# Kernel tuning notes

Hardware: AMD Instinct MI355X
Metric: run time of the kernel (lower is better)

The kernel has to match this reference:

```python
import jax, jax.numpy as jnp
import numpy as np

B = 4096
HID = 1024
Z1P = 256
Z1R = 256
Z2P = 128
Z2R = 128
N_STEP = 32


def _gru_cell(x, h, Wih, Whh, bih, bhh):
    # torch.nn.GRUCell math. Wih: [3H, in], Whh: [3H, H]
    gi = x @ Wih.T + bih  # [B, 3H]
    gh = h @ Whh.T + bhh  # [B, 3H]
    i_r, i_z, i_n = jnp.split(gi, 3, axis=1)
    h_r, h_z, h_n = jnp.split(gh, 3, axis=1)
    r = jax.nn.sigmoid(i_r + h_r)
    zg = jax.nn.sigmoid(i_z + h_z)
    n = jnp.tanh(i_n + r * h_n)
    return (1.0 - zg) * n + zg * h


def _decode(z, Wi, bi, Wih, Whh, bih, bhh, Wo, bo, out_dim):
    b = z.shape[0]
    h0 = jnp.tanh(z @ Wi.T + bi)  # linear_init + tanh
    out0 = jnp.zeros((b, out_dim), z.dtype).at[:, -1].set(1.0)  # SOS token

    def step(carry, _):
        out, h = carry
        x = jnp.concatenate([out, z], axis=1)  # [B, out_dim + z_dim]
        h = _gru_cell(x, h, Wih, Whh, bih, bhh)
        o = h @ Wo.T + bo  # linear_out
        return (o, h), o

    _, xs = jax.lax.scan(step, (out0, h0), None, length=N_STEP)  # xs: [T, B, out_dim]
    return jnp.transpose(xs, (1, 0, 2))  # [B, T, out_dim]


def setup_inputs() -> dict:
    key = jax.random.key(0)
    ks = jax.random.split(key, 24)
    s = lambda fan_in: 1.0 / np.sqrt(fan_in)
    u = lambda k, shape, fan_in: jax.random.uniform(k, shape, jnp.float32, -s(fan_in), s(fan_in))
    inp = {
        "z_8p": jax.random.normal(ks[0], (B, Z1P), jnp.float32),
        "z_8r": jax.random.normal(ks[1], (B, Z1R), jnp.float32),
        "z_4p": jax.random.normal(ks[2], (B, Z2P), jnp.float32),
        "z_4r": jax.random.normal(ks[3], (B, Z2R), jnp.float32),
        # linear_init_0 / linear_init_1
        "Wi0": u(ks[4], (HID, Z1P), Z1P), "bi0": u(ks[5], (HID,), Z1P),
        "Wi1": u(ks[6], (HID, Z1R), Z1R), "bi1": u(ks[7], (HID,), Z1R),
        # grucell_0 (input = z1p + z2p)
        "Wih0": u(ks[8], (3 * HID, Z1P + Z2P), HID), "Whh0": u(ks[9], (3 * HID, HID), HID),
        "bih0": u(ks[10], (3 * HID,), HID), "bhh0": u(ks[11], (3 * HID,), HID),
        # grucell_1 (input = z1r + z2r)
        "Wih1": u(ks[12], (3 * HID, Z1R + Z2R), HID), "Whh1": u(ks[13], (3 * HID, HID), HID),
        "bih1": u(ks[14], (3 * HID,), HID), "bhh1": u(ks[15], (3 * HID,), HID),
        # linear_out_0 / linear_out_1
        "Wo0": u(ks[16], (Z2P, HID), HID), "bo0": u(ks[17], (Z2P,), HID),
        "Wo1": u(ks[18], (Z2R, HID), HID), "bo1": u(ks[19], (Z2R,), HID),
    }
    return inp


def reference(z_8p, z_8r, z_4p, z_4r,
              Wi0, bi0, Wi1, bi1,
              Wih0, Whh0, bih0, bhh0,
              Wih1, Whh1, bih1, bhh1,
              Wo0, bo0, Wo1, bo1):
    # eval-mode forward; z_4p / z_4r are only cached during training and do not
    # affect the output (teacher-forcing branches in the source are no-ops).
    z4p = _decode(z_8p, Wi0, bi0, Wih0, Whh0, bih0, bhh0, Wo0, bo0, Z2P)
    z4r = _decode(z_8r, Wi1, bi1, Wih1, Whh1, bih1, bhh1, Wo1, bo1, Z2R)
    return (z4p, z4r)
```

## Files before the change

kernel.cpp:

```cpp
#include <hip/hip_runtime.h>
#include <stdint.h>


typedef unsigned short u16;
typedef __attribute__((ext_vector_type(8))) short bf8v;
typedef __attribute__((ext_vector_type(4))) float f4v;

constexpr int DECN = 2;
constexpr int BB = 4096;
constexpr int HH = 1024;
constexpr int ZZ = 256;
constexpr int OO = 128;
constexpr int TT = 32;
constexpr int GG = 3 * HH;
constexpr int WR = 4 * HH + OO;
constexpr int ILD = OO + ZZ;

__device__ __forceinline__ float bf2f(u16 u) {
  uint32_t x = ((uint32_t)u) << 16;
  return __builtin_bit_cast(float, x);
}
__device__ __forceinline__ u16 f2bf(float f) {
  uint32_t x = __builtin_bit_cast(uint32_t, f);
  x += 0x7fffu + ((x >> 16) & 1u);
  return (u16)(x >> 16);
}
__device__ __forceinline__ float sigf(float x) { return 1.f / (1.f + __expf(-x)); }
__device__ __forceinline__ float tanh_fast(float x) { return 2.f / (1.f + __expf(-2.f * x)) - 1.f; }

__device__ __forceinline__ void load16(const u16* g, u16* l) {
  __builtin_amdgcn_global_load_lds(
      (const __attribute__((address_space(1))) unsigned int*)g,
      (__attribute__((address_space(3))) unsigned int*)l, 16, 0, 0);
}

template <int NSEC>
__device__ __forceinline__ void gemm_core(
    const u16* __restrict__ A, int lda,
    const u16* __restrict__ Bm, int ldb,
    const int (&brow)[NSEC], int m0, int K,
    u16* Als, u16* Bls, f4v (&acc)[NSEC][4][2]) {
  const int tid = threadIdx.x;
  const int lane = tid & 63;
  const int wid = tid >> 6;
  const int wm = wid >> 1, wn = wid & 1;
  const int srow = lane >> 2;
  const int scol = (lane & 3) * 8;
  const int l15 = lane & 15;
  const int khalf = (lane >> 4) * 8;

  for (int k0 = 0; k0 < K; k0 += 32) {
    const u16* ga = A + (size_t)(m0 + wid * 16 + srow) * lda + k0 + scol;
    load16(ga, Als + (wid * 16) * 32);
    load16(ga + (size_t)64 * lda, Als + (64 + wid * 16) * 32);
#pragma unroll
    for (int s = 0; s < NSEC; ++s) {
      const u16* gb = Bm + (size_t)(brow[s] + wid * 16 + srow) * ldb + k0 + scol;
      load16(gb, Bls + (s * 64 + wid * 16) * 32);
    }
    __syncthreads();
    bf8v af[4];
#pragma unroll
    for (int mf = 0; mf < 4; ++mf)
      af[mf] = *(const bf8v*)(Als + (wm * 64 + mf * 16 + l15) * 32 + khalf);
#pragma unroll
    for (int s = 0; s < NSEC; ++s) {
#pragma unroll
      for (int nf = 0; nf < 2; ++nf) {
        bf8v bv = *(const bf8v*)(Bls + (s * 64 + wn * 32 + nf * 16 + l15) * 32 + khalf);
#pragma unroll
        for (int mf = 0; mf < 4; ++mf)
          acc[s][mf][nf] = __builtin_amdgcn_mfma_f32_16x16x32_bf16(af[mf], bv, acc[s][mf][nf], 0, 0, 0);
      }
    }
    __syncthreads();
  }
}


__global__ __launch_bounds__(256) void pack_kernel(const float* __restrict__ src, int ld, int col0,
                                                   u16* __restrict__ dst, int rows, int cols) {
  int i = blockIdx.x * 256 + threadIdx.x;
  if (i < rows * cols) {
    int r = i / cols, c = i - r * cols;
    dst[i] = f2bf(src[(size_t)r * ld + col0 + c]);
  }
}

__global__ __launch_bounds__(256) void wot_kernel(const float* __restrict__ wo, u16* __restrict__ dst) {
  int i = blockIdx.x * 256 + threadIdx.x;
  if (i < HH * OO) {
    int k = i / OO, c = i - k * OO;
    dst[i] = f2bf(wo[(size_t)c * HH + k]);
  }
}

__global__ __launch_bounds__(256) void vec_kernel(
    const float* __restrict__ wih0, const float* __restrict__ wih1,
    const float* __restrict__ bih0, const float* __restrict__ bih1,
    const float* __restrict__ bhh0, const float* __restrict__ bhh1,
    const float* __restrict__ bo0, const float* __restrict__ bo1,
    float* __restrict__ d1, float* __restrict__ v2) {
  int i = blockIdx.x * 256 + threadIdx.x;
  if (i >= DECN * GG) return;
  int dec = i / GG, j = i - dec * GG;
  const float* wih = dec ? wih1 : wih0;
  const float* bo = dec ? bo1 : bo0;
  const float* bih = dec ? bih1 : bih0;
  const float* bhh = dec ? bhh1 : bhh0;
  float bc = 0.f;
  for (int c = 0; c < OO; ++c) bc += wih[(size_t)j * ILD + c] * bo[c];
  d1[i] = wih[(size_t)j * ILD + (OO - 1)] - bc;
  v2[i] = bih[j] + (j < 2 * HH ? bhh[j] : 0.f) + bc;
}

__global__ __launch_bounds__(256, 2) void comb_kernel(
    const u16* __restrict__ wio, const u16* __restrict__ wot,
    const float* __restrict__ whh0, const float* __restrict__ whh1,
    u16* __restrict__ wb2) {
  __shared__ u16 Als[128 * 32];
  __shared__ u16 Bls[64 * 32];
  const int dec = blockIdx.z, m0 = blockIdx.x * 128, n0 = blockIdx.y * 64;
  const int lane = threadIdx.x & 63, wid = threadIdx.x >> 6;
  const int wm = wid >> 1, wn = wid & 1;
  const int rbase = m0 + wm * 64 + ((lane >> 4) << 2);
  const int clb = wn * 32 + (lane & 15);
  int brow[1] = {n0};
  f4v acc[1][4][2];
#pragma unroll
  for (int mf = 0; mf < 4; ++mf)
#pragma unroll
    for (int nf = 0; nf < 2; ++nf)
#pragma unroll
      for (int r = 0; r < 4; ++r) acc[0][mf][nf][r] = 0.f;
  gemm_core<1>(wio + (size_t)dec * GG * OO, OO, wot + (size_t)dec * HH * OO, OO, brow, m0, OO, Als, Bls, acc);
  const float* whh = dec ? whh1 : whh0;
  u16* W2 = wb2 + (size_t)dec * WR * HH;
#pragma unroll
  for (int mf = 0; mf < 4; ++mf)
#pragma unroll
    for (int nf = 0; nf < 2; ++nf) {
      const int k = n0 + clb + nf * 16;
#pragma unroll
      for (int r = 0; r < 4; ++r) {
        const int j = rbase + mf * 16 + r;
        float v = acc[0][mf][nf][r] + (j < 2 * HH ? whh[(size_t)j * HH + k] : 0.f);
        W2[(size_t)j * HH + k] = f2bf(v);
      }
    }
}

__global__ __launch_bounds__(256, 2) void gzc_kernel(
    const u16* __restrict__ zbf, const u16* __restrict__ wzb,
    const float* __restrict__ v2, u16* __restrict__ gzc) {
  __shared__ u16 Als[128 * 32];
  __shared__ u16 Bls[64 * 32];
  const int dec = blockIdx.z, m0 = blockIdx.x * 128, n0 = blockIdx.y * 64;
  const int lane = threadIdx.x & 63, wid = threadIdx.x >> 6;
  const int wm = wid >> 1, wn = wid & 1;
  const int rbase = m0 + wm * 64 + ((lane >> 4) << 2);
  const int clb = wn * 32 + (lane & 15);
  int brow[1] = {n0};
  f4v acc[1][4][2];
#pragma unroll
  for (int mf = 0; mf < 4; ++mf)
#pragma unroll
    for (int nf = 0; nf < 2; ++nf)
#pragma unroll
      for (int r = 0; r < 4; ++r) acc[0][mf][nf][r] = 0.f;
  gemm_core<1>(zbf + (size_t)dec * BB * ZZ, ZZ, wzb + (size_t)dec * GG * ZZ, ZZ, brow, m0, ZZ, Als, Bls, acc);
  const float* vv = v2 + dec * GG;
  u16* out = gzc + (size_t)dec * BB * GG;
#pragma unroll
  for (int mf = 0; mf < 4; ++mf)
#pragma unroll
    for (int nf = 0; nf < 2; ++nf) {
      const int col = n0 + clb + nf * 16;
#pragma unroll
      for (int r = 0; r < 4; ++r) {
        const int row = rbase + mf * 16 + r;
        out[(size_t)row * GG + col] = f2bf(acc[0][mf][nf][r] + vv[col]);
      }
    }
}

__global__ __launch_bounds__(256, 2) void h0_kernel(
    const u16* __restrict__ zbf, const u16* __restrict__ wib,
    const float* __restrict__ bi0, const float* __restrict__ bi1,
    float* __restrict__ hf, u16* __restrict__ hbf) {
  __shared__ u16 Als[128 * 32];
  __shared__ u16 Bls[64 * 32];
  const int dec = blockIdx.z, m0 = blockIdx.x * 128, n0 = blockIdx.y * 64;
  const int lane = threadIdx.x & 63, wid = threadIdx.x >> 6;
  const int wm = wid >> 1, wn = wid & 1;
  const int rbase = m0 + wm * 64 + ((lane >> 4) << 2);
  const int clb = wn * 32 + (lane & 15);
  int brow[1] = {n0};
  f4v acc[1][4][2];
#pragma unroll
  for (int mf = 0; mf < 4; ++mf)
#pragma unroll
    for (int nf = 0; nf < 2; ++nf)
#pragma unroll
      for (int r = 0; r < 4; ++r) acc[0][mf][nf][r] = 0.f;
  gemm_core<1>(zbf + (size_t)dec * BB * ZZ, ZZ, wib + (size_t)dec * HH * ZZ, ZZ, brow, m0, ZZ, Als, Bls, acc);
  const float* bi = dec ? bi1 : bi0;
  float* ho = hf + (size_t)dec * 2 * BB * HH;
  u16* hb = hbf + (size_t)dec * 2 * BB * HH;
#pragma unroll
  for (int mf = 0; mf < 4; ++mf)
#pragma unroll
    for (int nf = 0; nf < 2; ++nf) {
      const int col = n0 + clb + nf * 16;
#pragma unroll
      for (int r = 0; r < 4; ++r) {
        const int row = rbase + mf * 16 + r;
        float v = tanh_fast(acc[0][mf][nf][r] + bi[col]);
        ho[(size_t)row * HH + col] = v;
        hb[(size_t)row * HH + col] = f2bf(v);
      }
    }
}

__global__ __launch_bounds__(256, 2) void step_kernel(
    const u16* __restrict__ hbf_in, const float* __restrict__ hf_in,
    float* __restrict__ hf_out, u16* __restrict__ hbf_out,
    const u16* __restrict__ Wb, const u16* __restrict__ gzc,
    const float* __restrict__ d1,
    const float* __restrict__ bhh0v, const float* __restrict__ bhh1v,
    const float* __restrict__ bo0v, const float* __restrict__ bo1v,
    float* __restrict__ dout, int step1, int o_slot, int y_base) {
  __shared__ u16 Als[128 * 32];
  __shared__ u16 Bls[4 * 64 * 32];
  const int dec = blockIdx.z;
  const int ntile = blockIdx.y + y_base;
  const int m0 = blockIdx.x * 128;
  const int lane = threadIdx.x & 63, wid = threadIdx.x >> 6;
  const int wm = wid >> 1, wn = wid & 1;
  const int rbase = m0 + wm * 64 + ((lane >> 4) << 2);
  const int clb = wn * 32 + (lane & 15);
  const u16* A = hbf_in + (size_t)dec * 2 * BB * HH;
  const u16* W = Wb + (size_t)dec * WR * HH;

  if (ntile < 16) {
    const int j0 = ntile * 64;
    int brow[4] = {j0, HH + j0, 2 * HH + j0, 3 * HH + j0};
    const u16* gz = gzc + (size_t)dec * BB * GG;
    const float* dd = d1 + dec * GG;
    const float* bhhn = (dec ? bhh1v : bhh0v) + 2 * HH;
    f4v acc[4][4][2];
#pragma unroll
    for (int mf = 0; mf < 4; ++mf)
#pragma unroll
      for (int nf = 0; nf < 2; ++nf) {
        const int col = j0 + clb + nf * 16;
        const float dr0 = step1 ? dd[col] : 0.f;
        const float dr1 = step1 ? dd[HH + col] : 0.f;
        const float dr2 = step1 ? dd[2 * HH + col] : 0.f;
        const float bn = bhhn[col];
#pragma unroll
        for (int r = 0; r < 4; ++r) {
          const size_t ro = (size_t)(rbase + mf * 16 + r) * GG;
          acc[0][mf][nf][r] = bf2f(gz[ro + col]) + dr0;
          acc[1][mf][nf][r] = bf2f(gz[ro + HH + col]) + dr1;
          acc[2][mf][nf][r] = bf2f(gz[ro + 2 * HH + col]) + dr2;
          acc[3][mf][nf][r] = bn;
        }
      }
    gemm_core<4>(A, HH, W, HH, brow, m0, HH, Als, Bls, acc);
    const float* hold = hf_in + (size_t)dec * 2 * BB * HH;
    float* hnew = hf_out + (size_t)dec * 2 * BB * HH;
    u16* hnb = hbf_out + (size_t)dec * 2 * BB * HH;
#pragma unroll
    for (int mf = 0; mf < 4; ++mf)
#pragma unroll
      for (int nf = 0; nf < 2; ++nf) {
        const int col = j0 + clb + nf * 16;
#pragma unroll
        for (int r = 0; r < 4; ++r) {
          const int row = rbase + mf * 16 + r;
          float rg = sigf(acc[0][mf][nf][r]);
          float zg = sigf(acc[1][mf][nf][r]);
          float nn = tanh_fast(acc[2][mf][nf][r] + rg * acc[3][mf][nf][r]);
          float hv = hold[(size_t)row * HH + col];
          float hn = (1.f - zg) * nn + zg * hv;
          hnew[(size_t)row * HH + col] = hn;
          hnb[(size_t)row * HH + col] = f2bf(hn);
        }
      }
  } else {
    const int c0 = (ntile - 16) * 64;
    int brow[1] = {4 * HH + c0};
    const float* bod = dec ? bo1v : bo0v;
    f4v acc[1][4][2];
#pragma unroll
    for (int mf = 0; mf < 4; ++mf)
#pragma unroll
      for (int nf = 0; nf < 2; ++nf) {
        const float b = bod[c0 + clb + nf * 16];
#pragma unroll
        for (int r = 0; r < 4; ++r) acc[0][mf][nf][r] = b;
      }
    gemm_core<1>(A, HH, W, HH, brow, m0, HH, Als, Bls, acc);
    float* op = dout + (size_t)dec * BB * TT * OO + (size_t)o_slot * OO;
#pragma unroll
    for (int mf = 0; mf < 4; ++mf)
#pragma unroll
      for (int nf = 0; nf < 2; ++nf) {
        const int col = c0 + clb + nf * 16;
#pragma unroll
        for (int r = 0; r < 4; ++r) {
          const int row = rbase + mf * 16 + r;
          op[(size_t)row * TT * OO + col] = acc[0][mf][nf][r];
        }
      }
  }
}


extern "C" void kernel_launch(void* const* d_in, const int* in_sizes, int n_in,
                              void* d_out, int out_size, void* d_ws, size_t ws_size,
                              hipStream_t stream) {
  const float* z8[2] = {(const float*)d_in[0], (const float*)d_in[1]};
  const float* Wi[2] = {(const float*)d_in[4], (const float*)d_in[6]};
  const float* bi[2] = {(const float*)d_in[5], (const float*)d_in[7]};
  const float* Wih[2] = {(const float*)d_in[8], (const float*)d_in[12]};
  const float* Whh[2] = {(const float*)d_in[9], (const float*)d_in[13]};
  const float* bih[2] = {(const float*)d_in[10], (const float*)d_in[14]};
  const float* bhh[2] = {(const float*)d_in[11], (const float*)d_in[15]};
  const float* Wo[2] = {(const float*)d_in[16], (const float*)d_in[18]};
  const float* bo[2] = {(const float*)d_in[17], (const float*)d_in[19]};
  float* dout = (float*)d_out;

  char* p = (char*)d_ws;
  size_t off = 0;
  auto carve = [&](size_t nbytes) {
    char* r = p + off;
    off += (nbytes + 255) & ~(size_t)255;
    return (void*)r;
  };
  float* hf = (float*)carve((size_t)DECN * 2 * BB * HH * 4);
  u16* hbf = (u16*)carve((size_t)DECN * 2 * BB * HH * 2);
  u16* gzc = (u16*)carve((size_t)DECN * BB * GG * 2);
  u16* wb1 = (u16*)carve((size_t)DECN * WR * HH * 2);
  u16* wb2 = (u16*)carve((size_t)DECN * WR * HH * 2);
  u16* zbf = (u16*)carve((size_t)DECN * BB * ZZ * 2);
  u16* wzb = (u16*)carve((size_t)DECN * GG * ZZ * 2);
  u16* wio = (u16*)carve((size_t)DECN * GG * OO * 2);
  u16* wib = (u16*)carve((size_t)DECN * HH * ZZ * 2);
  u16* wot = (u16*)carve((size_t)DECN * HH * OO * 2);
  float* d1v = (float*)carve((size_t)DECN * GG * 4);
  float* v2v = (float*)carve((size_t)DECN * GG * 4);
  (void)ws_size; (void)in_sizes; (void)n_in; (void)out_size;

  auto pack = [&](const float* src, int ld, int c0, u16* dst, int rows, int cols) {
    int n = rows * cols;
    pack_kernel<<<(n + 255) / 256, 256, 0, stream>>>(src, ld, c0, dst, rows, cols);
  };
  for (int d = 0; d < 2; ++d) {
    pack(z8[d], ZZ, 0, zbf + (size_t)d * BB * ZZ, BB, ZZ);
    pack(Wih[d], ILD, OO, wzb + (size_t)d * GG * ZZ, GG, ZZ);
    pack(Wih[d], ILD, 0, wio + (size_t)d * GG * OO, GG, OO);
    pack(Wi[d], ZZ, 0, wib + (size_t)d * HH * ZZ, HH, ZZ);
    pack(Whh[d], HH, 0, wb1 + (size_t)d * WR * HH, 2 * HH, HH);
    pack(Whh[d] + (size_t)2 * HH * HH, HH, 0, wb1 + (size_t)d * WR * HH + (size_t)3 * HH * HH, HH, HH);
    pack(Whh[d] + (size_t)2 * HH * HH, HH, 0, wb2 + (size_t)d * WR * HH + (size_t)3 * HH * HH, HH, HH);
    pack(Wo[d], HH, 0, wb2 + (size_t)d * WR * HH + (size_t)4 * HH * HH, OO, HH);
    wot_kernel<<<(HH * OO + 255) / 256, 256, 0, stream>>>(Wo[d], wot + (size_t)d * HH * OO);
    hipMemsetAsync(wb1 + (size_t)d * WR * HH + (size_t)2 * HH * HH, 0, (size_t)HH * HH * 2, stream);
  }
  vec_kernel<<<(DECN * GG + 255) / 256, 256, 0, stream>>>(
      Wih[0], Wih[1], bih[0], bih[1], bhh[0], bhh[1], bo[0], bo[1], d1v, v2v);
  comb_kernel<<<dim3(24, 16, 2), 256, 0, stream>>>(wio, wot, Whh[0], Whh[1], wb2);
  gzc_kernel<<<dim3(32, 48, 2), 256, 0, stream>>>(zbf, wzb, v2v, gzc);
  h0_kernel<<<dim3(32, 16, 2), 256, 0, stream>>>(zbf, wib, bi[0], bi[1], hf, hbf);

  for (int t = 1; t <= TT; ++t) {
    const int bin = (t - 1) & 1, bout = t & 1;
    dim3 grid(32, t == 1 ? 16 : 18, 2);
    step_kernel<<<grid, 256, 0, stream>>>(
        hbf + (size_t)bin * BB * HH, hf + (size_t)bin * BB * HH,
        hf + (size_t)bout * BB * HH, hbf + (size_t)bout * BB * HH,
        t == 1 ? wb1 : wb2, gzc, d1v, bhh[0], bhh[1], bo[0], bo[1],
        dout, t == 1 ? 1 : 0, t - 2, 0);
  }
  step_kernel<<<dim3(32, 2, 2), 256, 0, stream>>>(
      hbf, hf, hf + (size_t)BB * HH, hbf + (size_t)BB * HH,
      wb2, gzc, d1v, bhh[0], bhh[1], bo[0], bo[1],
      dout, 0, TT - 1, 16);
}
```

Measured before the change: 3.427 ms.

## Replace step GEMM with 256-row, 8-wave, BK=64 double-buffered swizzled MFMA kernel

Replaces the per-step GRU kernel with a new 512-thread kernel that tiles 256 batch rows by four 64-column gate slices, using a 64-wide K tile. The loop double-buffers A and W tiles in LDS through direct global-to-LDS loads with an XOR swizzle. It interleaves prefetch with MFMA work using explicit waitcnt, barriers and setprio. The output projection is merged into one tile covering all 128 columns, and bias and gate-input addition move into the epilogue. This is meant to cut repeated weight and activation loads and raise MFMA utilisation, at the cost of fewer, larger blocks, higher register pressure and hand-tuned synchronisation that could be fragile.

Measured after the change: 3.209 ms. 6.4% less time.

```diff
diff --git a/kernel.cpp b/kernel.cpp
--- a/kernel.cpp
+++ b/kernel.cpp
@@ -15,6 +15,8 @@
 constexpr int GG = 3 * HH;
 constexpr int WR = 4 * HH + OO;
 constexpr int ILD = OO + ZZ;
+constexpr int BK = 64;
+constexpr int NKT = HH / BK;
 
 __device__ __forceinline__ float bf2f(u16 u) {
   uint32_t x = ((uint32_t)u) << 16;
@@ -222,7 +224,84 @@
     }
 }
 
-__global__ __launch_bounds__(256, 2) void step_kernel(
+template <int NS>
+__device__ __forceinline__ void kloop8(
+    const u16* __restrict__ A, const u16* __restrict__ W,
+    const int (&brow)[4], int m0, u16* lds, int lane, int wid,
+    f4v (&acc)[8][4]) {
+  const int wm = wid >> 2, wn = wid & 3;
+  const int l15 = lane & 15, lq = lane >> 4;
+  const int srow = wid * 8 + (lane >> 3);
+  const int sgc = (lane & 7) ^ ((lane >> 3) & 7);
+
+  auto stA = [&](int kt, int r) {
+    const u16* g = A + (size_t)(m0 + r * 64 + srow) * HH + kt * BK + sgc * 8;
+    load16(g, lds + ((kt & 1) * 2) * 16384 + (r * 64 + wid * 8) * 64);
+  };
+  auto stB = [&](int kt, int r) {
+    const u16* g = W + (size_t)(brow[r] + srow) * HH + kt * BK + sgc * 8;
+    load16(g, lds + ((kt & 1) * 2 + 1) * 16384 + (r * 64 + wid * 8) * 64);
+  };
+
+  stB(0, 0); stB(0, 1); stB(0, 2); stB(0, 3);
+  stA(0, 0); stA(0, 1); stA(0, 2); stA(0, 3);
+  asm volatile("s_waitcnt vmcnt(0)" ::: "memory");
+  __builtin_amdgcn_s_barrier();
+
+  auto tile = [&](int kt, bool pf) {
+    const u16* la = lds + (size_t)(kt & 1) * 32768;
+    const u16* lb = la + 16384;
+    bf8v bfr[NS][2];
+#pragma unroll
+    for (int q = 0; q < 4; ++q) {
+      if (q == 0) {
+#pragma unroll
+        for (int s = 0; s < NS; ++s)
+#pragma unroll
+          for (int ks = 0; ks < 2; ++ks)
+            bfr[s][ks] = *(const bf8v*)&lb[(s * 64 + wn * 16 + l15) * 64 +
+                                           (((ks * 4 + lq) ^ (l15 & 7)) * 8)];
+      }
+      bf8v aq[2][2];
+#pragma unroll
+      for (int mi = 0; mi < 2; ++mi)
+#pragma unroll
+        for (int ks = 0; ks < 2; ++ks)
+          aq[mi][ks] = *(const bf8v*)&la[(wm * 128 + (2 * q + mi) * 16 + l15) * 64 +
+                                         (((ks * 4 + lq) ^ (l15 & 7)) * 8)];
+      if (pf) {
+        if (q == 0) { stB(kt + 1, 0); stB(kt + 1, 1); }
+        if (q == 1) { stB(kt + 1, 2); stB(kt + 1, 3); }
+        if (q == 2) { stA(kt + 1, 0); stA(kt + 1, 2); }
+        if (q == 3) { stA(kt + 1, 1); stA(kt + 1, 3); }
+      }
+      __builtin_amdgcn_s_barrier();
+      asm volatile("s_waitcnt lgkmcnt(0)" ::: "memory");
+      __builtin_amdgcn_s_setprio(1);
+#pragma unroll
+      for (int mi = 0; mi < 2; ++mi)
+#pragma unroll
+        for (int s = 0; s < NS; ++s)
+#pragma unroll
+          for (int ks = 0; ks < 2; ++ks)
+            acc[2 * q + mi][s] = __builtin_amdgcn_mfma_f32_16x16x32_bf16(
+                aq[mi][ks], bfr[s][ks], acc[2 * q + mi][s], 0, 0, 0);
+      __builtin_amdgcn_s_setprio(0);
+      if (q == 1) {
+        if (pf) asm volatile("s_waitcnt vmcnt(4)" ::: "memory");
+        else    asm volatile("s_waitcnt vmcnt(0)" ::: "memory");
+      }
+      if (q == 3) {
+        asm volatile("s_waitcnt vmcnt(2)" ::: "memory");
+      }
+      __builtin_amdgcn_s_barrier();
+    }
+  };
+  for (int kt = 0; kt < NKT - 1; ++kt) tile(kt, true);
+  tile(NKT - 1, false);
+}
+
+__global__ __launch_bounds__(512, 2) void step8_kernel(
     const u16* __restrict__ hbf_in, const float* __restrict__ hf_in,
     float* __restrict__ hf_out, u16* __restrict__ hbf_out,
     const u16* __restrict__ Wb, const u16* __restrict__ gzc,
@@ -230,88 +309,73 @@
     const float* __restrict__ bhh0v, const float* __restrict__ bhh1v,
     const float* __restrict__ bo0v, const float* __restrict__ bo1v,
     float* __restrict__ dout, int step1, int o_slot, int y_base) {
-  __shared__ u16 Als[128 * 32];
-  __shared__ u16 Bls[4 * 64 * 32];
+  __shared__ u16 lds[4 * 16384];
   const int dec = blockIdx.z;
   const int ntile = blockIdx.y + y_base;
-  const int m0 = blockIdx.x * 128;
+  const int m0 = blockIdx.x * 256;
   const int lane = threadIdx.x & 63, wid = threadIdx.x >> 6;
-  const int wm = wid >> 1, wn = wid & 1;
-  const int rbase = m0 + wm * 64 + ((lane >> 4) << 2);
-  const int clb = wn * 32 + (lane & 15);
+  const int wm = wid >> 2, wn = wid & 3;
+  const int l15 = lane & 15, lq = lane >> 4;
   const u16* A = hbf_in + (size_t)dec * 2 * BB * HH;
   const u16* W = Wb + (size_t)dec * WR * HH;
+
+  f4v acc[8][4];
+#pragma unroll
+  for (int mf = 0; mf < 8; ++mf)
+#pragma unroll
+    for (int s = 0; s < 4; ++s)
+#pragma unroll
+      for (int r = 0; r < 4; ++r) acc[mf][s][r] = 0.f;
 
   if (ntile < 16) {
     const int j0 = ntile * 64;
     int brow[4] = {j0, HH + j0, 2 * HH + j0, 3 * HH + j0};
+    kloop8<4>(A, W, brow, m0, lds, lane, wid, acc);
+
     const u16* gz = gzc + (size_t)dec * BB * GG;
     const float* dd = d1 + dec * GG;
     const float* bhhn = (dec ? bhh1v : bhh0v) + 2 * HH;
-    f4v acc[4][4][2];
-#pragma unroll
-    for (int mf = 0; mf < 4; ++mf)
-#pragma unroll
-      for (int nf = 0; nf < 2; ++nf) {
-        const int col = j0 + clb + nf * 16;
-        const float dr0 = step1 ? dd[col] : 0.f;
-        const float dr1 = step1 ? dd[HH + col] : 0.f;
-        const float dr2 = step1 ? dd[2 * HH + col] : 0.f;
-        const float bn = bhhn[col];
-#pragma unroll
-        for (int r = 0; r < 4; ++r) {
-          const size_t ro = (size_t)(rbase + mf * 16 + r) * GG;
-          acc[0][mf][nf][r] = bf2f(gz[ro + col]) + dr0;
-          acc[1][mf][nf][r] = bf2f(gz[ro + HH + col]) + dr1;
-          acc[2][mf][nf][r] = bf2f(gz[ro + 2 * HH + col]) + dr2;
-          acc[3][mf][nf][r] = bn;
-        }
-      }
-    gemm_core<4>(A, HH, W, HH, brow, m0, HH, Als, Bls, acc);
     const float* hold = hf_in + (size_t)dec * 2 * BB * HH;
     float* hnew = hf_out + (size_t)dec * 2 * BB * HH;
     u16* hnb = hbf_out + (size_t)dec * 2 * BB * HH;
-#pragma unroll
-    for (int mf = 0; mf < 4; ++mf)
-#pragma unroll
-      for (int nf = 0; nf < 2; ++nf) {
-        const int col = j0 + clb + nf * 16;
+    const int col = j0 + wn * 16 + l15;
+    const float bn = bhhn[col];
+    const float dr0 = step1 ? dd[col] : 0.f;
+    const float dr1 = step1 ? dd[HH + col] : 0.f;
+    const float dr2 = step1 ? dd[2 * HH + col] : 0.f;
+#pragma unroll
+    for (int mf = 0; mf < 8; ++mf) {
+#pragma unroll
+      for (int r = 0; r < 4; ++r) {
+        const int row = m0 + wm * 128 + mf * 16 + lq * 4 + r;
+        const size_t ro = (size_t)row * GG;
+        float v0 = acc[mf][0][r] + bf2f(gz[ro + col]) + dr0;
+        float v1 = acc[mf][1][r] + bf2f(gz[ro + HH + col]) + dr1;
+        float v2 = acc[mf][2][r] + bf2f(gz[ro + 2 * HH + col]) + dr2;
+        float v3 = acc[mf][3][r] + bn;
+        float rg = sigf(v0), zg = sigf(v1);
+        float nn = tanh_fast(v2 + rg * v3);
+        float hv = hold[(size_t)row * HH + col];
+        float hn = (1.f - zg) * nn + zg * hv;
+        hnew[(size_t)row * HH + col] = hn;
+        hnb[(size_t)row * HH + col] = f2bf(hn);
+      }
+    }
+  } else {
+    int brow[4] = {4 * HH, 4 * HH + 64, 4 * HH, 4 * HH + 64};
+    kloop8<2>(A, W, brow, m0, lds, lane, wid, acc);
+    const float* bod = dec ? bo1v : bo0v;
+    float* op = dout + (size_t)dec * BB * TT * OO + (size_t)o_slot * OO;
+#pragma unroll
+    for (int mf = 0; mf < 8; ++mf)
+#pragma unroll
+      for (int s2 = 0; s2 < 2; ++s2) {
+        const int col = s2 * 64 + wn * 16 + l15;
+        const float b = bod[col];
 #pragma unroll
         for (int r = 0; r < 4; ++r) {
-          const int row = rbase + mf * 16 + r;
-          float rg = sigf(acc[0][mf][nf][r]);
-          float zg = sigf(acc[1][mf][nf][r]);
-          float nn = tanh_fast(acc[2][mf][nf][r] + rg * acc[3][mf][nf][r]);
-          float hv = hold[(size_t)row * HH + col];
-          float hn = (1.f - zg) * nn + zg * hv;
-          hnew[(size_t)row * HH + col] = hn;
-          hnb[(size_t)row * HH + col] = f2bf(hn);
-        }
-      }
-  } else {
-    const int c0 = (ntile - 16) * 64;
-    int brow[1] = {4 * HH + c0};
-    const float* bod = dec ? bo1v : bo0v;
-    f4v acc[1][4][2];
-#pragma unroll
-    for (int mf = 0; mf < 4; ++mf)
-#pragma unroll
-      for (int nf = 0; nf < 2; ++nf) {
-        const float b = bod[c0 + clb + nf * 16];
-#pragma unroll
-        for (int r = 0; r < 4; ++r) acc[0][mf][nf][r] = b;
-      }
-    gemm_core<1>(A, HH, W, HH, brow, m0, HH, Als, Bls, acc);
-    float* op = dout + (size_t)dec * BB * TT * OO + (size_t)o_slot * OO;
-#pragma unroll
-    for (int mf = 0; mf < 4; ++mf)
-#pragma unroll
-      for (int nf = 0; nf < 2; ++nf) {
-        const int col = c0 + clb + nf * 16;
-#pragma unroll
-        for (int r = 0; r < 4; ++r) {
-          const int row = rbase + mf * 16 + r;
-          op[(size_t)row * TT * OO + col] = acc[0][mf][nf][r];
+          const int row = m0 + wm * 128 + mf * 16 + lq * 4 + r;
+          op[(size_t)row * TT * OO + col] = acc[mf][s2][r] + b;
         }
       }
   }
@@ -377,14 +441,14 @@
 
   for (int t = 1; t <= TT; ++t) {
     const int bin = (t - 1) & 1, bout = t & 1;
-    dim3 grid(32, t == 1 ? 16 : 18, 2);
-    step_kernel<<<grid, 256, 0, stream>>>(
+    dim3 grid(16, t == 1 ? 16 : 17, 2);
+    step8_kernel<<<grid, 512, 0, stream>>>(
         hbf + (size_t)bin * BB * HH, hf + (size_t)bin * BB * HH,
         hf + (size_t)bout * BB * HH, hbf + (size_t)bout * BB * HH,
         t == 1 ? wb1 : wb2, gzc, d1v, bhh[0], bhh[1], bo[0], bo[1],
         dout, t == 1 ? 1 : 0, t - 2, 0);
   }
-  step_kernel<<<dim3(32, 2, 2), 256, 0, stream>>>(
+  step8_kernel<<<dim3(16, 1, 2), 512, 0, stream>>>(
       hbf, hf, hf + (size_t)BB * HH, hbf + (size_t)BB * HH,
       wb2, gzc, d1v, bhh[0], bhh[1], bo[0], bo[1],
       dout, 0, TT - 1, 16);
```
